# Optimization experiments

Measured on AMD Instinct MI355X. Metric: run time of the kernel, lower is better.

## Reference

```python
import jax, jax.numpy as jnp
import numpy as np

N, E, D = 50000, 800000, 128   # nodes, edges, input feature dim
HEADS, HC = 8, 16
H = HEADS * HC                 # 128 hidden width after concat
G, OUT = 64, 16                # graphs in batch, output classes
EPS_BN = 1e-5


def _gat_conv(x, src, dst, edge_attr, W, att_src, att_dst, We, att_edge, b):
    """PyG GATConv (concat=True, negative_slope=0.2, add_self_loops=True,
    fill_value='mean' for edge_attr, dropout inactive in eval)."""
    n = x.shape[0]
    # self-loop edge attr = per-node mean of incoming edge attrs
    ones = jnp.ones((src.shape[0], 1), x.dtype)
    deg = jax.ops.segment_sum(ones, dst, num_segments=n)
    ea_mean = jax.ops.segment_sum(edge_attr, dst, num_segments=n) / jnp.maximum(deg, 1.0)
    loop = jnp.arange(n, dtype=src.dtype)
    src_f = jnp.concatenate([src, loop])
    dst_f = jnp.concatenate([dst, loop])
    ea = jnp.concatenate([edge_attr, ea_mean])          # [E+N, 1]
    h = (x @ W).reshape(n, HEADS, HC)                   # [N, heads, hc]
    a_src = jnp.sum(h * att_src, axis=-1)               # [N, heads]
    a_dst = jnp.sum(h * att_dst, axis=-1)               # [N, heads]
    he = (ea @ We).reshape(-1, HEADS, HC)               # [E+N, heads, hc]
    a_e = jnp.sum(he * att_edge, axis=-1)               # [E+N, heads]
    alpha = jax.nn.leaky_relu(a_src[src_f] + a_dst[dst_f] + a_e, 0.2)
    # segment softmax over destination nodes
    amax = jax.ops.segment_max(alpha, dst_f, num_segments=n)
    ex = jnp.exp(alpha - amax[dst_f])
    denom = jax.ops.segment_sum(ex, dst_f, num_segments=n)
    coef = ex / (denom[dst_f] + 1e-16)                  # [E+N, heads]
    out = jax.ops.segment_sum(h[src_f] * coef[..., None], dst_f, num_segments=n)
    return out.reshape(n, H) + b


def setup_inputs() -> dict:
    key = jax.random.key(0)
    k = lambda i: jax.random.fold_in(key, i)
    nrm = lambda i, shape, s=0.1: jax.random.normal(k(i), shape, dtype=jnp.float32) * s
    inp = {
        "x": jax.random.normal(k(0), (N, D), dtype=jnp.float32),
        "edge_index": jax.random.randint(k(1), (2, E), 0, N, dtype=jnp.int32),
        "edge_weights": jax.random.normal(k(2), (E, 1), dtype=jnp.float32),
        "batch": jnp.sort(jax.random.randint(k(3), (N,), 0, G, dtype=jnp.int32)),
        "bn_gamma": jnp.ones((D,), jnp.float32),
        "bn_beta": jnp.zeros((D,), jnp.float32),
        "bn_mean": nrm(4, (D,)),
        "bn_var": jax.random.uniform(k(5), (D,), dtype=jnp.float32) + 0.5,
    }
    ci = 10
    for li, ind in [(1, D), (2, H), (3, H)]:
        inp[f"W{li}"] = nrm(ci, (ind, H)); ci += 1
        inp[f"att_src{li}"] = nrm(ci, (HEADS, HC)); ci += 1
        inp[f"att_dst{li}"] = nrm(ci, (HEADS, HC)); ci += 1
        inp[f"We{li}"] = nrm(ci, (1, H)); ci += 1
        inp[f"att_edge{li}"] = nrm(ci, (HEADS, HC)); ci += 1
        inp[f"b{li}"] = jnp.zeros((H,), jnp.float32)
    inp["Wl1"] = nrm(40, (H, 2 * HC)); inp["bl1"] = jnp.zeros((2 * HC,), jnp.float32)
    inp["Wl2"] = nrm(41, (2 * HC, OUT)); inp["bl2"] = jnp.zeros((OUT,), jnp.float32)
    return inp


def reference(x, edge_index, edge_weights, batch,
              bn_gamma, bn_beta, bn_mean, bn_var,
              W1, att_src1, att_dst1, We1, att_edge1, b1,
              W2, att_src2, att_dst2, We2, att_edge2, b2,
              W3, att_src3, att_dst3, We3, att_edge3, b3,
              Wl1, bl1, Wl2, bl2):
    src, dst = edge_index[0], edge_index[1]
    # BatchNorm (eval mode, running stats)
    h = (x - bn_mean) / jnp.sqrt(bn_var + EPS_BN) * bn_gamma + bn_beta
    h = jax.nn.relu(_gat_conv(h, src, dst, edge_weights, W1, att_src1, att_dst1, We1, att_edge1, b1))
    h = jax.nn.relu(_gat_conv(h, src, dst, edge_weights, W2, att_src2, att_dst2, We2, att_edge2, b2))
    h = _gat_conv(h, src, dst, edge_weights, W3, att_src3, att_dst3, We3, att_edge3, b3)
    g = jax.ops.segment_max(h, batch, num_segments=G)   # global max pool -> [G, H]
    g = jax.nn.relu(g @ Wl1 + bl1)
    # dropout p=0.5 is identity in eval mode
    return g @ Wl2 + bl2
```

## Files before the change

kernel.cpp:

```cpp
#include <hip/hip_runtime.h>
#include <math.h>

#define NN 50000
#define NE 800000
#define NH 8
#define HDIM 128
#define NG 64
#define PSPLIT 16
#define MAXD 64
#define GEMMB 782
#define SCATB 3125

typedef __attribute__((ext_vector_type(8))) short bf16x8;
typedef __attribute__((ext_vector_type(4))) float f32x4;

static __device__ __forceinline__ float lrelu02(float x){ return x > 0.f ? x : 0.2f*x; }
static __device__ __forceinline__ unsigned short f2bf(float f){
    unsigned u = __float_as_uint(f);
    unsigned r = (u + 0x7FFFu + ((u >> 16) & 1u)) >> 16;
    return (unsigned short)r;
}
static __device__ __forceinline__ float bf2f(unsigned short h){ return __uint_as_float((unsigned)h << 16); }
static __device__ __forceinline__ float bf_lo(unsigned v){ return __uint_as_float(v << 16); }
static __device__ __forceinline__ float bf_hi(unsigned v){ return __uint_as_float(v & 0xFFFF0000u); }

__global__ void k_prep0(const float* W1, const float* W2, const float* W3,
                        unsigned short* Wth, unsigned short* Wtl,
                        const float* We1, const float* ae1, const float* We2, const float* ae2,
                        const float* We3, const float* ae3, float* wev,
                        const float* gam, const float* bet, const float* mean, const float* var,
                        float* sc, float* sh, unsigned* cnt){
    if (blockIdx.x >= 193){
        int i = (blockIdx.x - 193)*256 + threadIdx.x;
        if (i < NN) cnt[i] = 0;
        return;
    }
    if (blockIdx.x == 192){
        int t = threadIdx.x;
        if (t < 128){
            float s = gam[t] * rsqrtf(var[t] + 1e-5f);
            sc[t] = s; sh[t] = bet[t] - mean[t] * s;
        } else if (t < 152){
            int q = t - 128; int l = q >> 3, hd = q & 7;
            const float* We = (l == 0) ? We1 : (l == 1) ? We2 : We3;
            const float* ae = (l == 0) ? ae1 : (l == 1) ? ae2 : ae3;
            float s = 0.f;
            for (int c = 0; c < 16; c++) s += We[hd*16+c] * ae[hd*16+c];
            wev[q] = s;
        }
        return;
    }
    int i = blockIdx.x*256 + threadIdx.x;
    int l = i >> 14, rem = i & 16383;
    int k = rem >> 7, n = rem & 127;
    const float* W = (l==0) ? W1 : (l==1) ? W2 : W3;
    float w = W[k*128 + n];
    unsigned short hi = f2bf(w);
    unsigned short lo = f2bf(w - bf2f(hi));
    Wth[l*16384 + n*128 + k] = hi;
    Wtl[l*16384 + n*128 + k] = lo;
}

__global__ __launch_bounds__(256, 3) void k_fused1(
        const int* srcp, const int* dstp, const float* ew, unsigned* cnt, unsigned* slab,
        const float* A, const unsigned short* Wth, const unsigned short* Wtl,
        const float* sc, const float* sh, const float* att_s, const float* att_d,
        unsigned* Hb, float* a_src, float* a_dst, int M){
    __shared__ unsigned short Ah[64][132];
    __shared__ unsigned short Al[64][132];
    if (blockIdx.x < SCATB){
        int i = blockIdx.x*256 + threadIdx.x;
        if (i >= NE) return;
        int d = dstp[i];
        float w = ew[i];
        unsigned rank = atomicAdd(&cnt[d], 1u);
        if (rank < MAXD){
            unsigned ent = (unsigned)srcp[i] | ((unsigned)f2bf(w) << 16);
            __builtin_nontemporal_store(ent, &slab[(size_t)d*MAXD + rank]);
        }
        return;
    }
    int t = threadIdx.x;
    int row0 = (blockIdx.x - SCATB) * 64;
    int w = t >> 6, l = t & 63;
    int lr = l & 15, lg = l >> 4;

    {
        const float2* A2 = (const float2*)A;
        for (int i = 0; i < 16; i++){
            int idx2 = t + i*256;
            int r = idx2 >> 6, c2 = idx2 & 63;
            float2 v = make_float2(0.f, 0.f);
            if (row0 + r < M){
                v = A2[(size_t)(row0+r)*64 + c2];
                float2 s2 = ((const float2*)sc)[c2], h2 = ((const float2*)sh)[c2];
                v.x = v.x*s2.x + h2.x; v.y = v.y*s2.y + h2.y;
            }
            unsigned short h0 = f2bf(v.x), h1 = f2bf(v.y);
            unsigned short l0 = f2bf(v.x - bf2f(h0)), l1 = f2bf(v.y - bf2f(h1));
            ((unsigned*)&Ah[r][0])[c2] = (unsigned)h0 | ((unsigned)h1 << 16);
            ((unsigned*)&Al[r][0])[c2] = (unsigned)l0 | ((unsigned)l1 << 16);
        }
    }
    __syncthreads();

    f32x4 acc[4][2];
    #pragma unroll
    for (int m = 0; m < 4; m++){ acc[m][0] = (f32x4){0,0,0,0}; acc[m][1] = (f32x4){0,0,0,0}; }

    #pragma unroll
    for (int ks = 0; ks < 4; ks++){
        int kk = ks*32 + lg*8;
        bf16x8 bh0 = *(const bf16x8*)&Wth[((w*2+0)*16 + lr)*128 + kk];
        bf16x8 bl0 = *(const bf16x8*)&Wtl[((w*2+0)*16 + lr)*128 + kk];
        bf16x8 bh1 = *(const bf16x8*)&Wth[((w*2+1)*16 + lr)*128 + kk];
        bf16x8 bl1 = *(const bf16x8*)&Wtl[((w*2+1)*16 + lr)*128 + kk];
        #pragma unroll
        for (int m = 0; m < 4; m++){
            bf16x8 a_h = *(const bf16x8*)&Ah[m*16 + lr][kk];
            bf16x8 a_l = *(const bf16x8*)&Al[m*16 + lr][kk];
            acc[m][0] = __builtin_amdgcn_mfma_f32_16x16x32_bf16(a_h, bh0, acc[m][0], 0, 0, 0);
            acc[m][0] = __builtin_amdgcn_mfma_f32_16x16x32_bf16(a_h, bl0, acc[m][0], 0, 0, 0);
            acc[m][0] = __builtin_amdgcn_mfma_f32_16x16x32_bf16(a_l, bh0, acc[m][0], 0, 0, 0);
            acc[m][1] = __builtin_amdgcn_mfma_f32_16x16x32_bf16(a_h, bh1, acc[m][1], 0, 0, 0);
            acc[m][1] = __builtin_amdgcn_mfma_f32_16x16x32_bf16(a_h, bl1, acc[m][1], 0, 0, 0);
            acc[m][1] = __builtin_amdgcn_mfma_f32_16x16x32_bf16(a_l, bh1, acc[m][1], 0, 0, 0);
        }
    }

    float asv[2], adv[2];
    #pragma unroll
    for (int n = 0; n < 2; n++){
        asv[n] = att_s[(w*2+n)*16 + lr];
        adv[n] = att_d[(w*2+n)*16 + lr];
    }
    #pragma unroll
    for (int m = 0; m < 4; m++){
        #pragma unroll
        for (int n = 0; n < 2; n++){
            #pragma unroll
            for (int r = 0; r < 4; r++){
                float v = acc[m][n][r];
                float pv = __shfl_xor(v, 1);
                int row = row0 + m*16 + lg*4 + r;
                if (!(l & 1) && row < M){
                    unsigned d = (unsigned)f2bf(v) | ((unsigned)f2bf(pv) << 16);
                    Hb[(size_t)row*64 + w*16 + n*8 + (lr >> 1)] = d;
                }
            }
        }
    }
    #pragma unroll
    for (int m = 0; m < 4; m++){
        #pragma unroll
        for (int r = 0; r < 4; r++){
            int row = row0 + m*16 + lg*4 + r;
            #pragma unroll
            for (int n = 0; n < 2; n++){
                float ps = acc[m][n][r] * asv[n];
                float pd = acc[m][n][r] * adv[n];
                #pragma unroll
                for (int off = 1; off < 16; off <<= 1){
                    ps += __shfl_xor(ps, off);
                    pd += __shfl_xor(pd, off);
                }
                if (lr == 0 && row < M){
                    a_src[row*NH + w*2 + n] = ps;
                    a_dst[row*NH + w*2 + n] = pd;
                }
            }
        }
    }
}

__global__ __launch_bounds__(256, 3) void k_gemm_bf(const unsigned* A16,
        const unsigned short* Wth, const unsigned short* Wtl,
        const float* att_s, const float* att_d,
        unsigned* Hb, float* a_src, float* a_dst, int M){
    __shared__ unsigned short Ah[64][132];
    int t = threadIdx.x;
    int row0 = blockIdx.x * 64;
    int w = t >> 6, l = t & 63;
    int lr = l & 15, lg = l >> 4;

    for (int i = 0; i < 16; i++){
        int idx = t + i*256;
        int r = idx >> 6, c2 = idx & 63;
        unsigned v = 0;
        if (row0 + r < M) v = A16[(size_t)(row0+r)*64 + c2];
        ((unsigned*)&Ah[r][0])[c2] = v;
    }
    __syncthreads();

    f32x4 acc[4][2];
    #pragma unroll
    for (int m = 0; m < 4; m++){ acc[m][0] = (f32x4){0,0,0,0}; acc[m][1] = (f32x4){0,0,0,0}; }

    #pragma unroll
    for (int ks = 0; ks < 4; ks++){
        int kk = ks*32 + lg*8;
        bf16x8 bh0 = *(const bf16x8*)&Wth[((w*2+0)*16 + lr)*128 + kk];
        bf16x8 bl0 = *(const bf16x8*)&Wtl[((w*2+0)*16 + lr)*128 + kk];
        bf16x8 bh1 = *(const bf16x8*)&Wth[((w*2+1)*16 + lr)*128 + kk];
        bf16x8 bl1 = *(const bf16x8*)&Wtl[((w*2+1)*16 + lr)*128 + kk];
        #pragma unroll
        for (int m = 0; m < 4; m++){
            bf16x8 a_h = *(const bf16x8*)&Ah[m*16 + lr][kk];
            acc[m][0] = __builtin_amdgcn_mfma_f32_16x16x32_bf16(a_h, bh0, acc[m][0], 0, 0, 0);
            acc[m][0] = __builtin_amdgcn_mfma_f32_16x16x32_bf16(a_h, bl0, acc[m][0], 0, 0, 0);
            acc[m][1] = __builtin_amdgcn_mfma_f32_16x16x32_bf16(a_h, bh1, acc[m][1], 0, 0, 0);
            acc[m][1] = __builtin_amdgcn_mfma_f32_16x16x32_bf16(a_h, bl1, acc[m][1], 0, 0, 0);
        }
    }

    float asv[2], adv[2];
    #pragma unroll
    for (int n = 0; n < 2; n++){
        asv[n] = att_s[(w*2+n)*16 + lr];
        adv[n] = att_d[(w*2+n)*16 + lr];
    }
    #pragma unroll
    for (int m = 0; m < 4; m++){
        #pragma unroll
        for (int n = 0; n < 2; n++){
            #pragma unroll
            for (int r = 0; r < 4; r++){
                float v = acc[m][n][r];
                float pv = __shfl_xor(v, 1);
                int row = row0 + m*16 + lg*4 + r;
                if (!(l & 1) && row < M){
                    unsigned d = (unsigned)f2bf(v) | ((unsigned)f2bf(pv) << 16);
                    Hb[(size_t)row*64 + w*16 + n*8 + (lr >> 1)] = d;
                }
            }
        }
    }
    #pragma unroll
    for (int m = 0; m < 4; m++){
        #pragma unroll
        for (int r = 0; r < 4; r++){
            int row = row0 + m*16 + lg*4 + r;
            #pragma unroll
            for (int n = 0; n < 2; n++){
                float ps = acc[m][n][r] * asv[n];
                float pd = acc[m][n][r] * adv[n];
                #pragma unroll
                for (int off = 1; off < 16; off <<= 1){
                    ps += __shfl_xor(ps, off);
                    pd += __shfl_xor(pd, off);
                }
                if (lr == 0 && row < M){
                    a_src[row*NH + w*2 + n] = ps;
                    a_dst[row*NH + w*2 + n] = pd;
                }
            }
        }
    }
}

__global__ __launch_bounds__(256) void k_aggr(const unsigned* cnt, const unsigned* slab,
                       const float* a_src, const float* a_dst, const float* wev,
                       const unsigned* Hb, const float* bias, unsigned* Out16, int do_relu){
    int wid = threadIdx.x >> 6, lane = threadIdx.x & 63;
    int n = blockIdx.x*4 + wid;
    if (n >= NN) return;
    unsigned dgt = cnt[n];
    int dg = (int)(dgt < MAXD ? dgt : MAXD);
    int hd = lane >> 3;
    int slot = lane >> 3;
    int headA = lane & 7;
    float adA = a_dst[n*NH + headA];
    float whA = wev[headA];
    unsigned vself = Hb[(size_t)n*64 + lane];
    float asnA = a_src[n*NH + headA];
    float accL0=0.f, accH0=0.f, accL1=0.f, accH1=0.f, den0=0.f, den1=0.f;
    float easumA = 0.f;
    const unsigned* srow = &slab[(size_t)n*MAXD];
    const uint4* srow4 = (const uint4*)srow;
    for (int base = 0; base < dg; base += 16){
        uint4 e0 = srow4[(base>>2)+0], e1 = srow4[(base>>2)+1];
        uint4 e2 = srow4[(base>>2)+2], e3 = srow4[(base>>2)+3];
        unsigned ent[16] = {e0.x,e0.y,e0.z,e0.w, e1.x,e1.y,e1.z,e1.w,
                            e2.x,e2.y,e2.z,e2.w, e3.x,e3.y,e3.z,e3.w};
        unsigned v[16];
        #pragma unroll
        for (int j = 0; j < 16; j++) v[j] = Hb[(size_t)(ent[j] & 0xFFFFu)*64 + lane];
        unsigned eA0 = srow[base + slot];
        unsigned eA1 = srow[base + 8 + slot];
        float ea0 = bf2f((unsigned short)(eA0 >> 16));
        float ea1 = bf2f((unsigned short)(eA1 >> 16));
        float as0 = a_src[(eA0 & 0xFFFFu)*NH + headA];
        float as1 = a_src[(eA1 & 0xFFFFu)*NH + headA];
        bool l0 = (base + slot) < dg, l1 = (base + 8 + slot) < dg;
        float c0 = l0 ? __expf(lrelu02(as0 + adA + ea0*whA)) : 0.f;
        float c1 = l1 ? __expf(lrelu02(as1 + adA + ea1*whA)) : 0.f;
        easumA += (l0 ? ea0 : 0.f) + (l1 ? ea1 : 0.f);
        #pragma unroll
        for (int j = 0; j < 8; j++){
            float cj = __shfl(c0, j*8 + hd);
            if (j & 1){ den1 += cj; accL1 += cj*bf_lo(v[j]); accH1 += cj*bf_hi(v[j]); }
            else      { den0 += cj; accL0 += cj*bf_lo(v[j]); accH0 += cj*bf_hi(v[j]); }
        }
        #pragma unroll
        for (int j = 0; j < 8; j++){
            float cj = __shfl(c1, j*8 + hd);
            if (j & 1){ den1 += cj; accL1 += cj*bf_lo(v[8+j]); accH1 += cj*bf_hi(v[8+j]); }
            else      { den0 += cj; accL0 += cj*bf_lo(v[8+j]); accH0 += cj*bf_hi(v[8+j]); }
        }
    }
    easumA += __shfl_xor(easumA, 8);
    easumA += __shfl_xor(easumA, 16);
    easumA += __shfl_xor(easumA, 32);
    float ea_self = easumA / fmaxf((float)dgt, 1.f);
    float csA = __expf(lrelu02(asnA + adA + ea_self*whA));
    float cs = __shfl(csA, hd);
    den0 += cs; accL0 += cs*bf_lo(vself); accH0 += cs*bf_hi(vself);
    float inv = 1.f / (den0 + den1 + 1e-16f);
    float2 bv = ((const float2*)bias)[lane];
    float o0 = (accL0 + accL1) * inv + bv.x;
    float o1 = (accH0 + accH1) * inv + bv.y;
    if (do_relu){ o0 = fmaxf(o0, 0.f); o1 = fmaxf(o1, 0.f); }
    Out16[(size_t)n*64 + lane] = (unsigned)f2bf(o0) | ((unsigned)f2bf(o1) << 16);
}

static __device__ int lower_bound_batch(const int* b, int v){
    int lo = 0, hi = NN;
    while (lo < hi){
        int mid = (lo + hi) >> 1;
        if (b[mid] < v) lo = mid + 1; else hi = mid;
    }
    return lo;
}

__global__ void k_pool1(const unsigned* A16, const int* batch, float* gpart){
    int g = blockIdx.x >> 4, s = blockIdx.x & (PSPLIT-1);
    int start = lower_bound_batch(batch, g);
    int end   = lower_bound_batch(batch, g + 1);
    int nrows = end - start;
    int chunk = (nrows + PSPLIT - 1) / PSPLIT;
    int rs = start + s*chunk;
    int re = rs + chunk; if (re > end) re = end;
    int c = threadIdx.x;
    float m0 = -INFINITY, m1 = -INFINITY;
    for (int r = rs; r < re; r++){
        unsigned v = A16[(size_t)r*64 + c];
        m0 = fmaxf(m0, bf_lo(v));
        m1 = fmaxf(m1, bf_hi(v));
    }
    ((float2*)&gpart[(size_t)blockIdx.x*HDIM])[c] = make_float2(m0, m1);
}

__global__ void k_pool2(const float* gpart, float* gp){
    int g = blockIdx.x, col = threadIdx.x;
    float m = -INFINITY;
    for (int s = 0; s < PSPLIT; s++)
        m = fmaxf(m, gpart[(size_t)(g*PSPLIT+s)*HDIM + col]);
    gp[g*HDIM + col] = m;
}

__global__ __launch_bounds__(256) void k_mlp(const float* gp, const float* Wl1, const float* bl1,
                      const float* Wl2, const float* bl2, float* out){
    __shared__ float gl[NG*HDIM];
    __shared__ float t1[NG*32];
    int t = threadIdx.x;
    for (int i = 0; i < 8; i++)
        ((float4*)gl)[t + i*256] = ((const float4*)gp)[t + i*256];
    __syncthreads();
    for (int i = 0; i < 8; i++){
        int o = t + i*256;
        int gi = o >> 5, j = o & 31;
        float s = bl1[j];
        for (int k = 0; k < 128; k++) s += gl[gi*128 + k] * Wl1[k*32 + j];
        t1[o] = fmaxf(s, 0.f);
    }
    __syncthreads();
    for (int i = 0; i < 4; i++){
        int o = t + i*256;
        int gi = o >> 4, j = o & 15;
        float s = bl2[j];
        for (int k = 0; k < 32; k++) s += t1[gi*32 + k] * Wl2[k*16 + j];
        out[o] = s;
    }
}

extern "C" void kernel_launch(void* const* d_in, const int* in_sizes, int n_in,
                              void* d_out, int out_size, void* d_ws, size_t ws_size,
                              hipStream_t stream){
    const float* x    = (const float*)d_in[0];
    const int*   ei   = (const int*)d_in[1];
    const float* ew   = (const float*)d_in[2];
    const int*   batch= (const int*)d_in[3];
    const float* bng  = (const float*)d_in[4];
    const float* bnb  = (const float*)d_in[5];
    const float* bnm  = (const float*)d_in[6];
    const float* bnv  = (const float*)d_in[7];
    const float* Wmat[3] = {(const float*)d_in[8],  (const float*)d_in[14], (const float*)d_in[20]};
    const float* asr[3]  = {(const float*)d_in[9],  (const float*)d_in[15], (const float*)d_in[21]};
    const float* adt[3]  = {(const float*)d_in[10], (const float*)d_in[16], (const float*)d_in[22]};
    const float* Wep[3]  = {(const float*)d_in[11], (const float*)d_in[17], (const float*)d_in[23]};
    const float* aep[3]  = {(const float*)d_in[12], (const float*)d_in[18], (const float*)d_in[24]};
    const float* bp[3]   = {(const float*)d_in[13], (const float*)d_in[19], (const float*)d_in[25]};
    const float* Wl1 = (const float*)d_in[26];
    const float* bl1 = (const float*)d_in[27];
    const float* Wl2 = (const float*)d_in[28];
    const float* bl2 = (const float*)d_in[29];

    char* p = (char*)d_ws;
    auto alloc = [&](size_t bytes)->char*{
        char* r = p; p += (bytes + 255) & ~(size_t)255; return r;
    };
    unsigned* Hb    = (unsigned*)alloc((size_t)NN*64*4);
    unsigned* A16   = (unsigned*)alloc((size_t)NN*64*4);
    float*    a_src = (float*)alloc((size_t)NN*NH*4);
    float*    a_dst = (float*)alloc((size_t)NN*NH*4);
    unsigned* cnt   = (unsigned*)alloc((size_t)NN*4);
    unsigned* slab  = (unsigned*)alloc((size_t)NN*MAXD*4);
    float*    wev   = (float*)alloc(24*4);
    float*    scv   = (float*)alloc(128*4);
    float*    shv   = (float*)alloc(128*4);
    unsigned short* Wth = (unsigned short*)alloc((size_t)3*16384*2);
    unsigned short* Wtl = (unsigned short*)alloc((size_t)3*16384*2);
    float*    gpart = (float*)alloc((size_t)NG*PSPLIT*HDIM*4);
    float*    gpool = (float*)alloc((size_t)NG*HDIM*4);

    const int* srcp = ei;
    const int* dstp = ei + NE;

    k_prep0<<<193 + 196, 256, 0, stream>>>(Wmat[0], Wmat[1], Wmat[2], Wth, Wtl,
                                     Wep[0], aep[0], Wep[1], aep[1], Wep[2], aep[2], wev,
                                     bng, bnb, bnm, bnv, scv, shv, cnt);
    k_fused1<<<SCATB + GEMMB, 256, 0, stream>>>(srcp, dstp, ew, cnt, slab,
                                            x, Wth, Wtl, scv, shv,
                                            asr[0], adt[0], Hb, a_src, a_dst, NN);
    k_aggr<<<(NN+3)/4, 256, 0, stream>>>(cnt, slab, a_src, a_dst, wev,
                                         Hb, bp[0], A16, 1);
    for (int l = 1; l < 3; l++){
        k_gemm_bf<<<(NN+63)/64, 256, 0, stream>>>(A16, Wth + l*16384, Wtl + l*16384,
                                                  asr[l], adt[l], Hb, a_src, a_dst, NN);
        k_aggr<<<(NN+3)/4, 256, 0, stream>>>(cnt, slab, a_src, a_dst, wev + l*8,
                                             Hb, bp[l], A16, (l < 2) ? 1 : 0);
    }
    k_pool1<<<NG*PSPLIT, 64, 0, stream>>>(A16, batch, gpart);
    k_pool2<<<NG, 128, 0, stream>>>(gpart, gpool);
    k_mlp<<<1, 256, 0, stream>>>(gpool, Wl1, bl1, Wl2, bl2, (float*)d_out);
}
```

Baseline: 318.9 us.

## Split fused scatter/GEMM kernel and fold pool reduction into MLP

```diff
diff --git a/kernel.cpp b/kernel.cpp
--- a/kernel.cpp
+++ b/kernel.cpp
@@ -8,8 +8,6 @@
 #define NG 64
 #define PSPLIT 16
 #define MAXD 64
-#define GEMMB 782
-#define SCATB 3125
 
 typedef __attribute__((ext_vector_type(8))) short bf16x8;
 typedef __attribute__((ext_vector_type(4))) float f32x4;
@@ -61,27 +59,28 @@
     Wtl[l*16384 + n*128 + k] = lo;
 }
 
-__global__ __launch_bounds__(256, 3) void k_fused1(
-        const int* srcp, const int* dstp, const float* ew, unsigned* cnt, unsigned* slab,
-        const float* A, const unsigned short* Wth, const unsigned short* Wtl,
-        const float* sc, const float* sh, const float* att_s, const float* att_d,
+__global__ void k_scatter(const int* srcp, const int* dstp, const float* ew,
+                          unsigned* cnt, unsigned* slab){
+    int i = blockIdx.x*256 + threadIdx.x;
+    if (i >= NE) return;
+    int d = dstp[i];
+    float w = ew[i];
+    unsigned rank = atomicAdd(&cnt[d], 1u);
+    if (rank < MAXD){
+        unsigned ent = (unsigned)srcp[i] | ((unsigned)f2bf(w) << 16);
+        __builtin_nontemporal_store(ent, &slab[(size_t)d*MAXD + rank]);
+    }
+}
+
+__global__ __launch_bounds__(256, 3) void k_gemm1(const float* A,
+        const unsigned short* Wth, const unsigned short* Wtl,
+        const float* sc, const float* sh,
+        const float* att_s, const float* att_d,
         unsigned* Hb, float* a_src, float* a_dst, int M){
     __shared__ unsigned short Ah[64][132];
     __shared__ unsigned short Al[64][132];
-    if (blockIdx.x < SCATB){
-        int i = blockIdx.x*256 + threadIdx.x;
-        if (i >= NE) return;
-        int d = dstp[i];
-        float w = ew[i];
-        unsigned rank = atomicAdd(&cnt[d], 1u);
-        if (rank < MAXD){
-            unsigned ent = (unsigned)srcp[i] | ((unsigned)f2bf(w) << 16);
-            __builtin_nontemporal_store(ent, &slab[(size_t)d*MAXD + rank]);
-        }
-        return;
-    }
     int t = threadIdx.x;
-    int row0 = (blockIdx.x - SCATB) * 64;
+    int row0 = blockIdx.x * 64;
     int w = t >> 6, l = t & 63;
     int lr = l & 15, lg = l >> 4;
 
@@ -350,21 +349,19 @@
     ((float2*)&gpart[(size_t)blockIdx.x*HDIM])[c] = make_float2(m0, m1);
 }
 
-__global__ void k_pool2(const float* gpart, float* gp){
-    int g = blockIdx.x, col = threadIdx.x;
-    float m = -INFINITY;
-    for (int s = 0; s < PSPLIT; s++)
-        m = fmaxf(m, gpart[(size_t)(g*PSPLIT+s)*HDIM + col]);
-    gp[g*HDIM + col] = m;
-}
-
-__global__ __launch_bounds__(256) void k_mlp(const float* gp, const float* Wl1, const float* bl1,
+__global__ __launch_bounds__(256) void k_mlp(const float* gpart, const float* Wl1, const float* bl1,
                       const float* Wl2, const float* bl2, float* out){
     __shared__ float gl[NG*HDIM];
     __shared__ float t1[NG*32];
     int t = threadIdx.x;
-    for (int i = 0; i < 8; i++)
-        ((float4*)gl)[t + i*256] = ((const float4*)gp)[t + i*256];
+    for (int i = 0; i < 32; i++){
+        int o = t + i*256;
+        int g = o >> 7, col = o & 127;
+        float m = -INFINITY;
+        for (int s = 0; s < PSPLIT; s++)
+            m = fmaxf(m, gpart[(size_t)(g*PSPLIT+s)*HDIM + col]);
+        gl[o] = m;
+    }
     __syncthreads();
     for (int i = 0; i < 8; i++){
         int o = t + i*256;
@@ -421,7 +418,6 @@
     unsigned short* Wth = (unsigned short*)alloc((size_t)3*16384*2);
     unsigned short* Wtl = (unsigned short*)alloc((size_t)3*16384*2);
     float*    gpart = (float*)alloc((size_t)NG*PSPLIT*HDIM*4);
-    float*    gpool = (float*)alloc((size_t)NG*HDIM*4);
 
     const int* srcp = ei;
     const int* dstp = ei + NE;
@@ -429,8 +425,9 @@
     k_prep0<<<193 + 196, 256, 0, stream>>>(Wmat[0], Wmat[1], Wmat[2], Wth, Wtl,
                                      Wep[0], aep[0], Wep[1], aep[1], Wep[2], aep[2], wev,
                                      bng, bnb, bnm, bnv, scv, shv, cnt);
-    k_fused1<<<SCATB + GEMMB, 256, 0, stream>>>(srcp, dstp, ew, cnt, slab,
-                                            x, Wth, Wtl, scv, shv,
+    k_scatter<<<(NE+255)/256, 256, 0, stream>>>(srcp, dstp, ew, cnt, slab);
+
+    k_gemm1<<<(NN+63)/64, 256, 0, stream>>>(x, Wth, Wtl, scv, shv,
                                             asr[0], adt[0], Hb, a_src, a_dst, NN);
     k_aggr<<<(NN+3)/4, 256, 0, stream>>>(cnt, slab, a_src, a_dst, wev,
                                          Hb, bp[0], A16, 1);
@@ -441,6 +438,5 @@
                                              Hb, bp[l], A16, (l < 2) ? 1 : 0);
     }
     k_pool1<<<NG*PSPLIT, 64, 0, stream>>>(A16, batch, gpart);
-    k_pool2<<<NG, 128, 0, stream>>>(gpart, gpool);
-    k_mlp<<<1, 256, 0, stream>>>(gpool, Wl1, bl1, Wl2, bl2, (float*)d_out);
-}
+    k_mlp<<<1, 256, 0, stream>>>(gpart, Wl1, bl1, Wl2, bl2, (float*)d_out);
+}
```

Measured after the change: 313.4 us. About the same (-1.7%).
